# Kernel tuning notes

Hardware: AMD Instinct MI355X
Metric: run time of the kernel (lower is better)

## Reference

```python
import jax, jax.numpy as jnp
import numpy as np


def _feature_map(x):
    # elu(x) + 1, the canonical positive feature map for linear attention
    return jax.nn.elu(x) + 1.0


def setup_inputs() -> dict:
    key = jax.random.key(0)
    kq, kk, kv = jax.random.split(key, 3)
    B, T, H, D, M = 2, 2048, 8, 64, 64
    q = jax.random.normal(kq, (B, T, H, D), dtype=jnp.float32)
    k = jax.random.normal(kk, (B, T, H, D), dtype=jnp.float32)
    v = jax.random.normal(kv, (B, T, H, M), dtype=jnp.float32)
    return {"q": q, "k": k, "v": v}


def reference(q, k, v):
    # q,k: [B,T,H,D]; v: [B,T,H,M]
    qf = _feature_map(q)
    kf = _feature_map(k)
    # running sum of keys over time (causal)
    k_sum = jnp.cumsum(kf, axis=1)                      # [B,T,H,D]
    z = 1.0 / jnp.einsum('bthd,bthd->bth', qf, k_sum)   # [B,T,H]
    # outer products k_i v_i^T; NOTE: original torch code cumsums over dim=-2
    # (the D axis of the [B,T,H,D,M] tensor), reproduced faithfully here.
    kv = jnp.einsum('bthd,bthm->bthdm', kf, v)           # [B,T,H,D,M]
    kv_sum = jnp.cumsum(kv, axis=-2)                     # cumsum over D, per source
    out = jnp.einsum('bthd,bthdm,bth->bthm', qf, kv_sum, z)
    return out
```

## Files before the change

### kernel.cpp

```cpp
#include <hip/hip_runtime.h>

#define BB 2
#define TT 2048
#define HH 8
#define DD 64
#define CC 256
#define TC (TT / CC)
#define STRIDE (HH * DD)
#define NBH (BB * HH)
#define CPW (CC / 16)

__device__ __forceinline__ float feat(float x) {
    return x > 0.f ? x + 1.f : __expf(x);
}

__device__ __forceinline__ void feat4(float4& a) {
    a.x = feat(a.x); a.y = feat(a.y); a.z = feat(a.z); a.w = feat(a.w);
}

__device__ __forceinline__ void xorred4(float4& a) {
    a.x += __shfl_xor(a.x, 16, 64); a.y += __shfl_xor(a.y, 16, 64);
    a.z += __shfl_xor(a.z, 16, 64); a.w += __shfl_xor(a.w, 16, 64);
    a.x += __shfl_xor(a.x, 32, 64); a.y += __shfl_xor(a.y, 32, 64);
    a.z += __shfl_xor(a.z, 32, 64); a.w += __shfl_xor(a.w, 32, 64);
}


__global__ void __launch_bounds__(1024)
scan_kernel(const float* __restrict__ k, float* __restrict__ ws) {
    const int bh   = blockIdx.x;
    const int w    = threadIdx.x >> 6;
    const int lane = threadIdx.x & 63;
    const int g    = lane & 15;
    const int seg  = lane >> 4;

    const int b = bh >> 3, h = bh & 7;
    const size_t base = (((size_t)b * TT + w * CPW * TC + seg) * HH + h) * DD + g * 4;

    float4 excl[CPW];
    float4 run = make_float4(0.f, 0.f, 0.f, 0.f);
    #pragma unroll 4
    for (int i = 0; i < CPW; ++i) {
        const size_t o0 = base + (size_t)(i * TC) * STRIDE;
        float4 a = *(const float4*)(k + o0);
        float4 c = *(const float4*)(k + o0 + (size_t)4 * STRIDE);
        float4 s;
        s.x = feat(a.x) + feat(c.x);
        s.y = feat(a.y) + feat(c.y);
        s.z = feat(a.z) + feat(c.z);
        s.w = feat(a.w) + feat(c.w);
        xorred4(s);
        excl[i] = run;
        run.x += s.x; run.y += s.y; run.z += s.z; run.w += s.w;
    }

    __shared__ float tot[16][DD];
    if (seg == 0)
        *(float4*)(&tot[w][g * 4]) = run;
    __syncthreads();

    float4 carry = make_float4(0.f, 0.f, 0.f, 0.f);
    for (int w2 = 0; w2 < w; ++w2) {
        const float4 t = *(const float4*)(&tot[w2][g * 4]);
        carry.x += t.x; carry.y += t.y; carry.z += t.z; carry.w += t.w;
    }

    if (seg == 0) {
        float* wsb = ws + ((size_t)bh * CC + w * CPW) * DD + g * 4;
        #pragma unroll
        for (int i = 0; i < CPW; ++i) {
            float4 e;
            e.x = excl[i].x + carry.x; e.y = excl[i].y + carry.y;
            e.z = excl[i].z + carry.z; e.w = excl[i].w + carry.w;
            *(float4*)(wsb + (size_t)i * DD) = e;
        }
    }
}

__global__ void __launch_bounds__(64)
linattn_kernel(const float* __restrict__ q, const float* __restrict__ k,
               const float* __restrict__ v, const float* __restrict__ ws,
               float* __restrict__ out) {
    const int idx  = blockIdx.x;
    const int c    = idx & (CC - 1);
    const int h    = (idx >> 8) & (HH - 1);
    const int b    = idx >> 11;
    const int lane = threadIdx.x;
    const int g    = lane & 15;
    const int seg  = lane >> 4;

    const size_t off0 = (((size_t)b * TT + c * TC + seg) * HH + h) * DD + g * 4;
    const size_t off1 = off0 + (size_t)4 * STRIDE;

    float4 kf0 = *(const float4*)(k + off0);
    float4 kf1 = *(const float4*)(k + off1);
    float4 qf0 = *(const float4*)(q + off0);
    float4 qf1 = *(const float4*)(q + off1);
    const float4 vv0 = *(const float4*)(v + off0);
    const float4 vv1 = *(const float4*)(v + off1);
    const float4 carry = *(const float4*)(ws + (size_t)idx * DD + g * 4);

    feat4(kf0); feat4(kf1); feat4(qf0); feat4(qf1);

    float4 i0 = kf0, i1 = kf1;
    {
        float u;
        u = __shfl_up(i0.x, 16, 64); if (seg >= 1) i0.x += u;
        u = __shfl_up(i0.y, 16, 64); if (seg >= 1) i0.y += u;
        u = __shfl_up(i0.z, 16, 64); if (seg >= 1) i0.z += u;
        u = __shfl_up(i0.w, 16, 64); if (seg >= 1) i0.w += u;
        u = __shfl_up(i1.x, 16, 64); if (seg >= 1) i1.x += u;
        u = __shfl_up(i1.y, 16, 64); if (seg >= 1) i1.y += u;
        u = __shfl_up(i1.z, 16, 64); if (seg >= 1) i1.z += u;
        u = __shfl_up(i1.w, 16, 64); if (seg >= 1) i1.w += u;
        u = __shfl_up(i0.x, 32, 64); if (seg >= 2) i0.x += u;
        u = __shfl_up(i0.y, 32, 64); if (seg >= 2) i0.y += u;
        u = __shfl_up(i0.z, 32, 64); if (seg >= 2) i0.z += u;
        u = __shfl_up(i0.w, 32, 64); if (seg >= 2) i0.w += u;
        u = __shfl_up(i1.x, 32, 64); if (seg >= 2) i1.x += u;
        u = __shfl_up(i1.y, 32, 64); if (seg >= 2) i1.y += u;
        u = __shfl_up(i1.z, 32, 64); if (seg >= 2) i1.z += u;
        u = __shfl_up(i1.w, 32, 64); if (seg >= 2) i1.w += u;
    }
    float4 S0;
    S0.x = __shfl(i0.x, 48 + g, 64);
    S0.y = __shfl(i0.y, 48 + g, 64);
    S0.z = __shfl(i0.z, 48 + g, 64);
    S0.w = __shfl(i0.w, 48 + g, 64);

    float4 run0, run1;
    run0.x = carry.x + i0.x; run0.y = carry.y + i0.y;
    run0.z = carry.z + i0.z; run0.w = carry.w + i0.w;
    run1.x = carry.x + S0.x + i1.x; run1.y = carry.y + S0.y + i1.y;
    run1.z = carry.z + S0.z + i1.z; run1.w = carry.w + S0.w + i1.w;

    float4 p0, p1;
    p0.x = kf0.x; p0.y = p0.x + kf0.y; p0.z = p0.y + kf0.z; p0.w = p0.z + kf0.w;
    p1.x = kf1.x; p1.y = p1.x + kf1.y; p1.z = p1.y + kf1.z; p1.w = p1.z + kf1.w;
    float c0 = p0.w, c1 = p1.w;
    #pragma unroll
    for (int o = 1; o <= 8; o <<= 1) {
        float u0 = __shfl_up(c0, o, 16);
        float u1 = __shfl_up(c1, o, 16);
        if (g >= o) { c0 += u0; c1 += u1; }
    }
    const float e0 = c0 - p0.w;
    const float e1 = c1 - p1.w;

    const float sq0 = qf0.x + qf0.y + qf0.z + qf0.w;
    const float sq1 = qf1.x + qf1.y + qf1.z + qf1.w;
    float s1_0 = qf0.x * p0.x + qf0.y * p0.y + qf0.z * p0.z + qf0.w * p0.w + e0 * sq0;
    float s2_0 = qf0.x * run0.x + qf0.y * run0.y + qf0.z * run0.z + qf0.w * run0.w;
    float s1_1 = qf1.x * p1.x + qf1.y * p1.y + qf1.z * p1.z + qf1.w * p1.w + e1 * sq1;
    float s2_1 = qf1.x * run1.x + qf1.y * run1.y + qf1.z * run1.z + qf1.w * run1.w;
    #pragma unroll
    for (int o = 1; o <= 8; o <<= 1) {
        s1_0 += __shfl_xor(s1_0, o, 64);
        s2_0 += __shfl_xor(s2_0, o, 64);
        s1_1 += __shfl_xor(s1_1, o, 64);
        s2_1 += __shfl_xor(s2_1, o, 64);
    }

    const float r0 = s1_0 * __builtin_amdgcn_rcpf(s2_0);
    const float r1 = s1_1 * __builtin_amdgcn_rcpf(s2_1);
    float4 o0, o1;
    o0.x = vv0.x * r0; o0.y = vv0.y * r0; o0.z = vv0.z * r0; o0.w = vv0.w * r0;
    o1.x = vv1.x * r1; o1.y = vv1.y * r1; o1.z = vv1.z * r1; o1.w = vv1.w * r1;
    *(float4*)(out + off0) = o0;
    *(float4*)(out + off1) = o1;
}

extern "C" void kernel_launch(void* const* d_in, const int* in_sizes, int n_in,
                              void* d_out, int out_size, void* d_ws, size_t ws_size,
                              hipStream_t stream) {
    const float* q = (const float*)d_in[0];
    const float* k = (const float*)d_in[1];
    const float* v = (const float*)d_in[2];
    float* out = (float*)d_out;
    float* ws  = (float*)d_ws;

    scan_kernel<<<NBH, 1024, 0, stream>>>(k, ws);
    linattn_kernel<<<BB * HH * CC, 64, 0, stream>>>(q, k, v, ws, out);
}
```

Baseline: 94.32 us.

## Split key prefix scan into 16 group blocks per head with deferred carry

The key-sum scan previously ran one 1024-thread block per batch-head, with each wave walking 16 chunks serially. It now launches 16 blocks per batch-head, each scanning only 16 chunks and writing per-chunk exclusive sums plus a per-group total. The main kernel then adds the totals of earlier groups into its carry, so the scan is spread across far more CUs. The cost is extra global reads and a cross-lane reduction in every attention block.

```diff
diff --git a/kernel.cpp b/kernel.cpp
--- a/kernel.cpp
+++ b/kernel.cpp
@@ -8,7 +8,8 @@
 #define TC (TT / CC)
 #define STRIDE (HH * DD)
 #define NBH (BB * HH)
-#define CPW (CC / 16)
+#define NG 16
+#define GS_OFF ((size_t)NBH * CC * DD)
 
 __device__ __forceinline__ float feat(float x) {
     return x > 0.f ? x + 1.f : __expf(x);
@@ -27,52 +28,48 @@
 
 
 __global__ void __launch_bounds__(1024)
-scan_kernel(const float* __restrict__ k, float* __restrict__ ws) {
-    const int bh   = blockIdx.x;
+group_scan_kernel(const float* __restrict__ k, float* __restrict__ ws) {
+    const int blk  = blockIdx.x;
+    const int g16  = blk & (NG - 1);
+    const int bh   = blk >> 4;
     const int w    = threadIdx.x >> 6;
     const int lane = threadIdx.x & 63;
     const int g    = lane & 15;
     const int seg  = lane >> 4;
+    const int b    = bh >> 3, h = bh & 7;
+    const int c    = g16 * 16 + w;
 
-    const int b = bh >> 3, h = bh & 7;
-    const size_t base = (((size_t)b * TT + w * CPW * TC + seg) * HH + h) * DD + g * 4;
+    const size_t off0 = (((size_t)b * TT + c * TC + seg) * HH + h) * DD + g * 4;
+    float4 k0 = *(const float4*)(k + off0);
+    float4 k1 = *(const float4*)(k + off0 + (size_t)4 * STRIDE);
+    feat4(k0); feat4(k1);
 
-    float4 excl[CPW];
-    float4 run = make_float4(0.f, 0.f, 0.f, 0.f);
-    #pragma unroll 4
-    for (int i = 0; i < CPW; ++i) {
-        const size_t o0 = base + (size_t)(i * TC) * STRIDE;
-        float4 a = *(const float4*)(k + o0);
-        float4 c = *(const float4*)(k + o0 + (size_t)4 * STRIDE);
-        float4 s;
-        s.x = feat(a.x) + feat(c.x);
-        s.y = feat(a.y) + feat(c.y);
-        s.z = feat(a.z) + feat(c.z);
-        s.w = feat(a.w) + feat(c.w);
-        xorred4(s);
-        excl[i] = run;
-        run.x += s.x; run.y += s.y; run.z += s.z; run.w += s.w;
-    }
+    float4 s;
+    s.x = k0.x + k1.x; s.y = k0.y + k1.y;
+    s.z = k0.z + k1.z; s.w = k0.w + k1.w;
+    xorred4(s);
 
     __shared__ float tot[16][DD];
     if (seg == 0)
-        *(float4*)(&tot[w][g * 4]) = run;
+        *(float4*)(&tot[w][g * 4]) = s;
     __syncthreads();
 
-    float4 carry = make_float4(0.f, 0.f, 0.f, 0.f);
-    for (int w2 = 0; w2 < w; ++w2) {
+    float4 ex = make_float4(0.f, 0.f, 0.f, 0.f);
+    for (int w2 = seg; w2 < w; w2 += 4) {
         const float4 t = *(const float4*)(&tot[w2][g * 4]);
-        carry.x += t.x; carry.y += t.y; carry.z += t.z; carry.w += t.w;
+        ex.x += t.x; ex.y += t.y; ex.z += t.z; ex.w += t.w;
     }
+    xorred4(ex);
 
+    float* chunkE = ws;
+    float* groupS = ws + GS_OFF;
     if (seg == 0) {
-        float* wsb = ws + ((size_t)bh * CC + w * CPW) * DD + g * 4;
-        #pragma unroll
-        for (int i = 0; i < CPW; ++i) {
-            float4 e;
-            e.x = excl[i].x + carry.x; e.y = excl[i].y + carry.y;
-            e.z = excl[i].z + carry.z; e.w = excl[i].w + carry.w;
-            *(float4*)(wsb + (size_t)i * DD) = e;
+        *(float4*)(chunkE + ((size_t)bh * CC + c) * DD + g * 4) = ex;
+        if (w == 15) {
+            float4 gt;
+            gt.x = ex.x + s.x; gt.y = ex.y + s.y;
+            gt.z = ex.z + s.z; gt.w = ex.w + s.w;
+            *(float4*)(groupS + ((size_t)bh * NG + g16) * DD + g * 4) = gt;
         }
     }
 }
@@ -85,6 +82,7 @@
     const int c    = idx & (CC - 1);
     const int h    = (idx >> 8) & (HH - 1);
     const int b    = idx >> 11;
+    const int bh   = idx >> 8;
     const int lane = threadIdx.x;
     const int g    = lane & 15;
     const int seg  = lane >> 4;
@@ -98,7 +96,21 @@
     float4 qf1 = *(const float4*)(q + off1);
     const float4 vv0 = *(const float4*)(v + off0);
     const float4 vv1 = *(const float4*)(v + off1);
-    const float4 carry = *(const float4*)(ws + (size_t)idx * DD + g * 4);
+
+    const float* chunkE = ws;
+    const float* groupS = ws + GS_OFF;
+    float4 carry = make_float4(0.f, 0.f, 0.f, 0.f);
+    const int ngp = c >> 4;
+    const float* gsb = groupS + ((size_t)bh * NG) * DD + g * 4;
+    for (int gp = seg; gp < ngp; gp += 4) {
+        const float4 t = *(const float4*)(gsb + (size_t)gp * DD);
+        carry.x += t.x; carry.y += t.y; carry.z += t.z; carry.w += t.w;
+    }
+    xorred4(carry);
+    {
+        const float4 e = *(const float4*)(chunkE + (size_t)idx * DD + g * 4);
+        carry.x += e.x; carry.y += e.y; carry.z += e.z; carry.w += e.w;
+    }
 
     feat4(kf0); feat4(kf1); feat4(qf0); feat4(qf1);
 
@@ -179,6 +191,6 @@
     float* out = (float*)d_out;
     float* ws  = (float*)d_ws;
 
-    scan_kernel<<<NBH, 1024, 0, stream>>>(k, ws);
+    group_scan_kernel<<<NBH * NG, 1024, 0, stream>>>(k, ws);
     linattn_kernel<<<BB * HH * CC, 64, 0, stream>>>(q, k, v, ws, out);
 }
```

Result: faster. 81.28 us (-13.8%).
